# Kernel tuning notes

Measured on AMD Instinct MI355X. Metric: run time of the kernel, lower is better.

The kernel has to match this reference:

```python
import jax, jax.numpy as jnp
import numpy as np

N = 100000   # nodes
E = 3200000  # edges
F = 128      # input features
H1 = 128     # first_gcn_dimensions
H2 = 64      # second_gcn_dimensions
D1 = 64      # first_dense_neurons
D2 = 8       # second_dense_neurons
L = 10       # number_of_labels


def setup_inputs() -> dict:
    key = jax.random.key(0)
    ks = jax.random.split(key, 8)
    edges = jax.random.randint(ks[0], (2, E), 0, N)
    features = jax.random.normal(ks[1], (N, F), dtype=jnp.float32)
    s = lambda k, shape: jax.random.normal(k, shape, dtype=jnp.float32) * 0.05
    return dict(
        edges=edges, features=features,
        W1=s(ks[2], (F, H1)), b1=jnp.zeros((H1,), jnp.float32),
        W2=s(ks[3], (H1, H2)), b2=jnp.zeros((H2,), jnp.float32),
        Wf1=s(ks[4], (H2, D1)), bf1=jnp.zeros((D1,), jnp.float32),
        Wf2=s(ks[5], (D1, D2)), bf2=jnp.zeros((D2,), jnp.float32),
        Wl=s(ks[6], (H2 * D2, L)), bl=jnp.zeros((L,), jnp.float32),
    )


def gcn_conv(x, W, b, src, dst, n):
    # PyG GCNConv: x' = D^{-1/2} (A + I) D^{-1/2} (x W) + b  (self-loops already in src/dst)
    h = x @ W                                            # [N, out]
    deg = jax.ops.segment_sum(jnp.ones(dst.shape[0], x.dtype), dst, num_segments=n)
    dinv = jnp.where(deg > 0, jax.lax.rsqrt(deg), 0.0)   # deg^{-1/2}, 0 for isolated
    norm = dinv[src] * dinv[dst]                         # [E+N]
    agg = jax.ops.segment_sum(h[src] * norm[:, None], dst, num_segments=n)
    return agg + b


def reference(edges, features, W1, b1, W2, b2, Wf1, bf1, Wf2, bf2, Wl, bl):
    n = features.shape[0]
    loop = jnp.arange(n)
    src = jnp.concatenate([edges[0], loop])
    dst = jnp.concatenate([edges[1], loop])

    h1 = jax.nn.relu(gcn_conv(features, W1, b1, src, dst, n))  # [N, H1]
    h2 = gcn_conv(h1, W2, b2, src, dst, n)                     # [N, H2]

    a1 = jnp.tanh(h2 @ Wf1 + bf1)                              # [N, D1]
    att = jax.nn.softmax(a1 @ Wf2 + bf2, axis=0)               # softmax over nodes, [N, D2]

    graph_embedding = (att.T @ h2).reshape(1, -1)              # [1, D2*H2]
    P = att.T @ att - jnp.eye(att.shape[1], dtype=att.dtype)   # [D2, D2]
    penalty = jnp.sum(jnp.sqrt(jnp.sum(P * P, axis=1)))

    predictions = jax.nn.log_softmax(graph_embedding @ Wl + bl, axis=1)  # [1, L]
    return graph_embedding, penalty, predictions
```

## Files before the change

kernel.cpp:

```cpp
#include <hip/hip_runtime.h>
#include <hip/hip_bf16.h>
#include <math.h>

#define NNODES 100000
#define NEDGES 3200000
#define NBUK ((NNODES + 127) >> 7)
#define NCHUNK 256
#define EPC (NEDGES / NCHUNK)

typedef float floatx2 __attribute__((ext_vector_type(2)));
typedef float f32x4 __attribute__((ext_vector_type(4)));
typedef short bf16x8 __attribute__((ext_vector_type(8)));

__device__ __forceinline__ unsigned short f2bf(float x) {
    unsigned u = __float_as_uint(x);
    unsigned r = u + 0x7FFFu + ((u >> 16) & 1u);
    return (unsigned short)(r >> 16);
}

__device__ __forceinline__ void acc8_fp8(uint2 v, floatx2* a) {
    a[0] += __builtin_amdgcn_cvt_pk_f32_fp8(v.x, false);
    a[1] += __builtin_amdgcn_cvt_pk_f32_fp8(v.x, true);
    a[2] += __builtin_amdgcn_cvt_pk_f32_fp8(v.y, false);
    a[3] += __builtin_amdgcn_cvt_pk_f32_fp8(v.y, true);
}

__global__ void prep_w_kernel(const float* __restrict__ W1, const float* __restrict__ W2,
                              unsigned short* __restrict__ Wt1, unsigned short* __restrict__ Wt2) {
    int i = blockIdx.x * 256 + threadIdx.x;
    if (i < 128 * 128) {
        int k = i >> 7, n = i & 127;
        Wt1[n * 128 + k] = f2bf(W1[i]);
    } else if (i < 128 * 128 + 128 * 64) {
        int j = i - 128 * 128;
        int k = j >> 6, n = j & 63;
        Wt2[n * 128 + k] = f2bf(W2[j]);
    }
}

__global__ __launch_bounds__(1024) void chunk_hist_kernel(const int* __restrict__ dst,
                                                          int* __restrict__ hist) {
    __shared__ int h[NBUK];
    int c = blockIdx.x, t = threadIdx.x;
    for (int i = t; i < NBUK; i += 1024) h[i] = 0;
    __syncthreads();
    const int4* d4 = (const int4*)(dst + c * EPC);
    for (int i = t; i < EPC / 4; i += 1024) {
        int4 d = d4[i];
        atomicAdd(&h[d.x >> 7], 1);
        atomicAdd(&h[d.y >> 7], 1);
        atomicAdd(&h[d.z >> 7], 1);
        atomicAdd(&h[d.w >> 7], 1);
    }
    __syncthreads();
    for (int i = t; i < NBUK; i += 1024)
        hist[c * NBUK + i] = h[i];
}

__global__ __launch_bounds__(256) void col_scan_kernel(int* __restrict__ hist,
                                                       int* __restrict__ btot) {
    __shared__ int sdat[NCHUNK];
    int b = blockIdx.x;
    int t = threadIdx.x;
    int v = hist[t * NBUK + b];
    sdat[t] = v;
    __syncthreads();
#pragma unroll
    for (int off = 1; off < NCHUNK; off <<= 1) {
        int x = (t >= off) ? sdat[t - off] : 0;
        __syncthreads();
        sdat[t] += x;
        __syncthreads();
    }
    hist[t * NBUK + b] = sdat[t] - v;
    if (t == NCHUNK - 1) btot[b] = sdat[t];
}

__global__ void bucket_scan_kernel(const int* __restrict__ btot, int* __restrict__ bstart,
                                   int* __restrict__ row_start, float* __restrict__ smalls) {
    __shared__ int s[1024];
    int t = threadIdx.x;
    if (t < 592) smalls[t] = 0.0f;
    int v = (t < NBUK) ? btot[t] : 0;
    s[t] = v;
    __syncthreads();
    for (int off = 1; off < 1024; off <<= 1) {
        int x = (t >= off) ? s[t - off] : 0;
        __syncthreads();
        s[t] += x;
        __syncthreads();
    }
    if (t < NBUK) bstart[t] = s[t] - v;
    if (t == 0) {
        bstart[NBUK] = NEDGES;
        row_start[NNODES] = NEDGES;
    }
}

__global__ __launch_bounds__(1024) void chunk_scatter_kernel(const int* __restrict__ src,
                                                             const int* __restrict__ dst,
                                                             const int* __restrict__ hist,
                                                             const int* __restrict__ bstart,
                                                             int* __restrict__ ebuk) {
    __shared__ int cur[NBUK];
    int c = blockIdx.x, t = threadIdx.x;
    for (int i = t; i < NBUK; i += 1024)
        cur[i] = bstart[i] + hist[c * NBUK + i];
    __syncthreads();
    const int4* s4 = (const int4*)(src + c * EPC);
    const int4* d4 = (const int4*)(dst + c * EPC);
    for (int i = t; i < EPC / 4; i += 1024) {
        int4 s = s4[i];
        int4 d = d4[i];
        int p0 = atomicAdd(&cur[d.x >> 7], 1);
        ebuk[p0] = s.x | ((d.x & 127) << 20);
        int p1 = atomicAdd(&cur[d.y >> 7], 1);
        ebuk[p1] = s.y | ((d.y & 127) << 20);
        int p2 = atomicAdd(&cur[d.z >> 7], 1);
        ebuk[p2] = s.z | ((d.z & 127) << 20);
        int p3 = atomicAdd(&cur[d.w >> 7], 1);
        ebuk[p3] = s.w | ((d.w & 127) << 20);
    }
}

__global__ __launch_bounds__(256) void build_kernel(const int* __restrict__ ebuk,
                                                    const int* __restrict__ bstart,
                                                    int* __restrict__ row_start,
                                                    float* __restrict__ dinv,
                                                    int* __restrict__ csr) {
    __shared__ int cnt[128];
    __shared__ int scn[128];
    __shared__ int cur[128];
    int b = blockIdx.x;
    int t = threadIdx.x;
    int s0 = bstart[b], s1 = bstart[b + 1];
    if (t < 128) cnt[t] = 0;
    __syncthreads();
    for (int i = s0 + t; i < s1; i += 256)
        atomicAdd(&cnt[(ebuk[i] >> 20) & 127], 1);
    __syncthreads();
    if (t < 128) scn[t] = cnt[t];
    __syncthreads();
#pragma unroll
    for (int off = 1; off < 128; off <<= 1) {
        int x = (t < 128 && t >= off) ? scn[t - off] : 0;
        __syncthreads();
        if (t < 128) scn[t] += x;
        __syncthreads();
    }
    int node = b * 128 + t;
    if (t < 128) {
        int rs = s0 + scn[t] - cnt[t];
        cur[t] = rs;
        if (node < NNODES) {
            row_start[node] = rs;
            dinv[node] = rsqrtf((float)cnt[t] + 1.0f);
        }
    }
    __syncthreads();
    for (int i = s0 + t; i < s1; i += 256) {
        int v = ebuk[i];
        int pos = atomicAdd(&cur[(v >> 20) & 127], 1);
        csr[pos] = v & 0xFFFFF;
    }
}

template <int KIN, int KOUT, bool ABF16>
__global__ __launch_bounds__(256) void gemm_mfma_kernel(const void* __restrict__ Av,
                                                        const unsigned short* __restrict__ Wt,
                                                        const float* __restrict__ rowscale,
                                                        unsigned char* __restrict__ stage) {
    constexpr int LDK = KIN + 8;
    constexpr int LDC = KOUT + 4;
    constexpr int SH_AB = (64 + KOUT) * LDK * 2;
    constexpr int SH_C  = 64 * LDC * 4;
    constexpr int SH = SH_AB > SH_C ? SH_AB : SH_C;
    __shared__ char shbuf[SH];
    unsigned short* As = (unsigned short*)shbuf;
    unsigned short* Ws = As + 64 * LDK;
    float* Cs = (float*)shbuf;
    int t = threadIdx.x;
    int block_row = blockIdx.x * 64;

    for (int idx = t; idx < KOUT * (KIN / 8); idx += 256) {
        int n = idx / (KIN / 8), c = idx % (KIN / 8);
        *(uint4*)(Ws + n * LDK + c * 8) = *(const uint4*)(Wt + n * KIN + c * 8);
    }
    if (ABF16) {
        const unsigned short* A = (const unsigned short*)Av;
        for (int idx = t; idx < 64 * (KIN / 8); idx += 256) {
            int r = idx / (KIN / 8), c = idx % (KIN / 8);
            uint4 v = make_uint4(0, 0, 0, 0);
            if (block_row + r < NNODES)
                v = *(const uint4*)(A + (size_t)(block_row + r) * KIN + c * 8);
            *(uint4*)(As + r * LDK + c * 8) = v;
        }
    } else {
        const float* A = (const float*)Av;
        for (int idx = t; idx < 64 * (KIN / 4); idx += 256) {
            int r = idx / (KIN / 4), c = idx % (KIN / 4);
            float4 v = make_float4(0.f, 0.f, 0.f, 0.f);
            if (block_row + r < NNODES)
                v = *(const float4*)(A + (size_t)(block_row + r) * KIN + c * 4);
            unsigned p0 = (unsigned)f2bf(v.x) | ((unsigned)f2bf(v.y) << 16);
            unsigned p1 = (unsigned)f2bf(v.z) | ((unsigned)f2bf(v.w) << 16);
            *(uint2*)(As + r * LDK + c * 4) = make_uint2(p0, p1);
        }
    }
    __syncthreads();

    int wv = t >> 6, lane = t & 63;
    int r0 = wv * 16;
    int m = lane & 15, q = lane >> 4;
    constexpr int NT = KOUT / 16;
    constexpr int KS = KIN / 32;
    f32x4 acc[NT];
#pragma unroll
    for (int nt = 0; nt < NT; nt++) acc[nt] = (f32x4)(0.f);
    bf16x8 afr[KS];
#pragma unroll
    for (int ks = 0; ks < KS; ks++)
        afr[ks] = *(bf16x8*)(As + (r0 + m) * LDK + ks * 32 + q * 8);
#pragma unroll
    for (int nt = 0; nt < NT; nt++) {
#pragma unroll
        for (int ks = 0; ks < KS; ks++) {
            bf16x8 b = *(bf16x8*)(Ws + (nt * 16 + m) * LDK + ks * 32 + q * 8);
            acc[nt] = __builtin_amdgcn_mfma_f32_16x16x32_bf16(afr[ks], b, acc[nt], 0, 0, 0);
        }
    }
    __syncthreads();
#pragma unroll
    for (int nt = 0; nt < NT; nt++)
#pragma unroll
        for (int j = 0; j < 4; j++)
            Cs[(r0 + q * 4 + j) * LDC + nt * 16 + m] = acc[nt][j];
    __syncthreads();
    for (int idx = t; idx < 64 * (KOUT / 4); idx += 256) {
        int r = idx / (KOUT / 4), c4 = idx % (KOUT / 4);
        int row = block_row + r;
        if (row < NNODES) {
            float4 v = *(float4*)(Cs + r * LDC + c4 * 4);
            float d = rowscale[row];
            int pk = __builtin_amdgcn_cvt_pk_fp8_f32(v.x * d, v.y * d, 0, false);
            pk = __builtin_amdgcn_cvt_pk_fp8_f32(v.z * d, v.w * d, pk, true);
            *(unsigned*)(stage + (size_t)row * KOUT + c4 * 4) = (unsigned)pk;
        }
    }
}

__global__ __launch_bounds__(256) void gather128_kernel(
    const unsigned char* __restrict__ hs, const int* __restrict__ row_start,
    const int* __restrict__ csr, const float* __restrict__ dinv,
    const float* __restrict__ bias, unsigned short* __restrict__ out) {
    int wave = threadIdx.x >> 6;
    int lane = threadIdx.x & 63;
    int n = blockIdx.x * 4 + wave;
    if (n >= NNODES) return;
    int g = lane >> 4;
    int c = lane & 15;
    unsigned boff = (unsigned)c << 3;
    int start = row_start[n], end = row_start[n + 1];
    floatx2 acc[4];
#pragma unroll
    for (int i = 0; i < 4; i++) acc[i] = (floatx2)(0.f);
    int w = (start + 3) & ~3;
    if (w > end) w = end;
    {
        int e2 = start + g;
        if (e2 < w) {
            unsigned o = ((unsigned)csr[e2] << 7) + boff;
            acc8_fp8(*(const uint2*)(hs + o), acc);
        }
    }
    for (; w + 64 <= end; w += 64) {
        const int* cp = csr + w + 16 * g;
        int4 ca = *(const int4*)(cp);
        int4 cb = *(const int4*)(cp + 4);
        int4 cc = *(const int4*)(cp + 8);
        int4 cd = *(const int4*)(cp + 12);
        uint2 v0  = *(const uint2*)(hs + (((unsigned)ca.x << 7) + boff));
        uint2 v1  = *(const uint2*)(hs + (((unsigned)ca.y << 7) + boff));
        uint2 v2  = *(const uint2*)(hs + (((unsigned)ca.z << 7) + boff));
        uint2 v3  = *(const uint2*)(hs + (((unsigned)ca.w << 7) + boff));
        uint2 v4  = *(const uint2*)(hs + (((unsigned)cb.x << 7) + boff));
        uint2 v5  = *(const uint2*)(hs + (((unsigned)cb.y << 7) + boff));
        uint2 v6  = *(const uint2*)(hs + (((unsigned)cb.z << 7) + boff));
        uint2 v7  = *(const uint2*)(hs + (((unsigned)cb.w << 7) + boff));
        uint2 v8  = *(const uint2*)(hs + (((unsigned)cc.x << 7) + boff));
        uint2 v9  = *(const uint2*)(hs + (((unsigned)cc.y << 7) + boff));
        uint2 v10 = *(const uint2*)(hs + (((unsigned)cc.z << 7) + boff));
        uint2 v11 = *(const uint2*)(hs + (((unsigned)cc.w << 7) + boff));
        uint2 v12 = *(const uint2*)(hs + (((unsigned)cd.x << 7) + boff));
        uint2 v13 = *(const uint2*)(hs + (((unsigned)cd.y << 7) + boff));
        uint2 v14 = *(const uint2*)(hs + (((unsigned)cd.z << 7) + boff));
        uint2 v15 = *(const uint2*)(hs + (((unsigned)cd.w << 7) + boff));
        acc8_fp8(v0, acc);  acc8_fp8(v1, acc);  acc8_fp8(v2, acc);  acc8_fp8(v3, acc);
        acc8_fp8(v4, acc);  acc8_fp8(v5, acc);  acc8_fp8(v6, acc);  acc8_fp8(v7, acc);
        acc8_fp8(v8, acc);  acc8_fp8(v9, acc);  acc8_fp8(v10, acc); acc8_fp8(v11, acc);
        acc8_fp8(v12, acc); acc8_fp8(v13, acc); acc8_fp8(v14, acc); acc8_fp8(v15, acc);
    }
    for (; w + 16 <= end; w += 16) {
        int4 cs = *(const int4*)(csr + w + 4 * g);
        uint2 v0 = *(const uint2*)(hs + (((unsigned)cs.x << 7) + boff));
        uint2 v1 = *(const uint2*)(hs + (((unsigned)cs.y << 7) + boff));
        uint2 v2 = *(const uint2*)(hs + (((unsigned)cs.z << 7) + boff));
        uint2 v3 = *(const uint2*)(hs + (((unsigned)cs.w << 7) + boff));
        acc8_fp8(v0, acc); acc8_fp8(v1, acc); acc8_fp8(v2, acc); acc8_fp8(v3, acc);
    }
    for (int e2 = w + g; e2 < end; e2 += 4) {
        unsigned o = ((unsigned)csr[e2] << 7) + boff;
        acc8_fp8(*(const uint2*)(hs + o), acc);
    }
#pragma unroll
    for (int off = 16; off <= 32; off <<= 1)
#pragma unroll
        for (int i = 0; i < 4; i++) {
            acc[i].x += __shfl_xor(acc[i].x, off);
            acc[i].y += __shfl_xor(acc[i].y, off);
        }
    if (g == 0) {
        floatx2 s[4];
#pragma unroll
        for (int i = 0; i < 4; i++) s[i] = (floatx2)(0.f);
        acc8_fp8(*(const uint2*)(hs + (((unsigned)n << 7) + boff)), s);
        float d = dinv[n];
        int j = c * 8;
        float4 b0 = *(const float4*)(bias + j);
        float4 b1 = *(const float4*)(bias + j + 4);
        float r0 = fmaxf((acc[0].x + s[0].x) * d + b0.x, 0.f);
        float r1 = fmaxf((acc[0].y + s[0].y) * d + b0.y, 0.f);
        float r2 = fmaxf((acc[1].x + s[1].x) * d + b0.z, 0.f);
        float r3 = fmaxf((acc[1].y + s[1].y) * d + b0.w, 0.f);
        float r4 = fmaxf((acc[2].x + s[2].x) * d + b1.x, 0.f);
        float r5 = fmaxf((acc[2].y + s[2].y) * d + b1.y, 0.f);
        float r6 = fmaxf((acc[3].x + s[3].x) * d + b1.z, 0.f);
        float r7 = fmaxf((acc[3].y + s[3].y) * d + b1.w, 0.f);
        uint4 p;
        p.x = (unsigned)f2bf(r0) | ((unsigned)f2bf(r1) << 16);
        p.y = (unsigned)f2bf(r2) | ((unsigned)f2bf(r3) << 16);
        p.z = (unsigned)f2bf(r4) | ((unsigned)f2bf(r5) << 16);
        p.w = (unsigned)f2bf(r6) | ((unsigned)f2bf(r7) << 16);
        *(uint4*)(out + (((size_t)n << 7) + j)) = p;
    }
}

__global__ __launch_bounds__(256) void gather64_kernel(
    const unsigned char* __restrict__ hs, const int* __restrict__ row_start,
    const int* __restrict__ csr, const float* __restrict__ dinv,
    const float* __restrict__ bias, float* __restrict__ out) {
    int wave = threadIdx.x >> 6;
    int lane = threadIdx.x & 63;
    int n = blockIdx.x * 4 + wave;
    if (n >= NNODES) return;
    int g = lane >> 3;
    int c = lane & 7;
    unsigned boff = (unsigned)c << 3;
    int start = row_start[n], end = row_start[n + 1];
    floatx2 acc[4];
#pragma unroll
    for (int i = 0; i < 4; i++) acc[i] = (floatx2)(0.f);
    int w = (start + 3) & ~3;
    if (w > end) w = end;
    {
        int e2 = start + g;
        if (e2 < w) {
            unsigned o = ((unsigned)csr[e2] << 6) + boff;
            acc8_fp8(*(const uint2*)(hs + o), acc);
        }
    }
    for (; w + 64 <= end; w += 64) {
        const int* cp = csr + w + 8 * g;
        int4 ca = *(const int4*)(cp);
        int4 cb = *(const int4*)(cp + 4);
        uint2 v0 = *(const uint2*)(hs + (((unsigned)ca.x << 6) + boff));
        uint2 v1 = *(const uint2*)(hs + (((unsigned)ca.y << 6) + boff));
        uint2 v2 = *(const uint2*)(hs + (((unsigned)ca.z << 6) + boff));
        uint2 v3 = *(const uint2*)(hs + (((unsigned)ca.w << 6) + boff));
        uint2 v4 = *(const uint2*)(hs + (((unsigned)cb.x << 6) + boff));
        uint2 v5 = *(const uint2*)(hs + (((unsigned)cb.y << 6) + boff));
        uint2 v6 = *(const uint2*)(hs + (((unsigned)cb.z << 6) + boff));
        uint2 v7 = *(const uint2*)(hs + (((unsigned)cb.w << 6) + boff));
        acc8_fp8(v0, acc); acc8_fp8(v1, acc); acc8_fp8(v2, acc); acc8_fp8(v3, acc);
        acc8_fp8(v4, acc); acc8_fp8(v5, acc); acc8_fp8(v6, acc); acc8_fp8(v7, acc);
    }
    for (; w + 16 <= end; w += 16) {
        int2 cs = *(const int2*)(csr + w + 2 * g);
        uint2 v0 = *(const uint2*)(hs + (((unsigned)cs.x << 6) + boff));
        uint2 v1 = *(const uint2*)(hs + (((unsigned)cs.y << 6) + boff));
        acc8_fp8(v0, acc); acc8_fp8(v1, acc);
    }
    for (int e2 = w + g; e2 < end; e2 += 8) {
        unsigned o = ((unsigned)csr[e2] << 6) + boff;
        acc8_fp8(*(const uint2*)(hs + o), acc);
    }
#pragma unroll
    for (int off = 8; off <= 32; off <<= 1)
#pragma unroll
        for (int i = 0; i < 4; i++) {
            acc[i].x += __shfl_xor(acc[i].x, off);
            acc[i].y += __shfl_xor(acc[i].y, off);
        }
    if (g == 0) {
        floatx2 s[4];
#pragma unroll
        for (int i = 0; i < 4; i++) s[i] = (floatx2)(0.f);
        acc8_fp8(*(const uint2*)(hs + (((unsigned)n << 6) + boff)), s);
        float d = dinv[n];
        int j = c * 8;
        float4 b0 = *(const float4*)(bias + j);
        float4 b1 = *(const float4*)(bias + j + 4);
        float4 o0, o1;
        o0.x = (acc[0].x + s[0].x) * d + b0.x;
        o0.y = (acc[0].y + s[0].y) * d + b0.y;
        o0.z = (acc[1].x + s[1].x) * d + b0.z;
        o0.w = (acc[1].y + s[1].y) * d + b0.w;
        o1.x = (acc[2].x + s[2].x) * d + b1.x;
        o1.y = (acc[2].y + s[2].y) * d + b1.y;
        o1.z = (acc[3].x + s[3].x) * d + b1.z;
        o1.w = (acc[3].y + s[3].y) * d + b1.w;
        float* op = out + (((size_t)n << 6) + j);
        *(float4*)op = o0;
        *(float4*)(op + 4) = o1;
    }
}

__global__ __launch_bounds__(256) void attnpool_kernel(const float* __restrict__ h2,
                                                       const float* __restrict__ Wf1,
                                                       const float* __restrict__ bf1,
                                                       const float* __restrict__ Wf2,
                                                       const float* __restrict__ bf2,
                                                       float* __restrict__ ge,
                                                       float* __restrict__ ata,
                                                       float* __restrict__ colsum) {
    __shared__ float h2S[64][68];
    __shared__ float a1S[64][68];
    __shared__ float attS[64][8];
    __shared__ float colS[8][64];
    int t = threadIdx.x;
    int d0 = t >> 6;
    int j  = t & 63;
    int de = t >> 3, ee = t & 7;
    float accge0 = 0.f, accge1 = 0.f, accata = 0.f, acccol = 0.f;
    int ntiles = (NNODES + 63) / 64;
    for (int tile = blockIdx.x; tile < ntiles; tile += gridDim.x) {
        int base = tile * 64;
#pragma unroll
        for (int q = 0; q < 4; q++) {
            int idx = t + q * 256;
            int r = idx >> 4, cc = (idx & 15) * 4;
            int row = base + r;
            float4 v = (row < NNODES) ? *(const float4*)(h2 + (size_t)row * 64 + cc)
                                      : make_float4(0.f, 0.f, 0.f, 0.f);
            *(float4*)(&h2S[r][cc]) = v;
        }
        __syncthreads();
        {
            int cg = t & 15, rg = t >> 4;
            int jj = cg * 4, r0 = rg * 4;
            float4 b4 = *(const float4*)(bf1 + jj);
            float4 acc[4];
#pragma unroll
            for (int r = 0; r < 4; r++) acc[r] = b4;
#pragma unroll 4
            for (int k = 0; k < 64; k++) {
                float4 wv = *(const float4*)(Wf1 + (size_t)k * 64 + jj);
#pragma unroll
                for (int r = 0; r < 4; r++) {
                    float a = h2S[r0 + r][k];
                    acc[r].x += a * wv.x; acc[r].y += a * wv.y;
                    acc[r].z += a * wv.z; acc[r].w += a * wv.w;
                }
            }
#pragma unroll
            for (int r = 0; r < 4; r++) {
                a1S[r0 + r][jj]     = tanhf(acc[r].x);
                a1S[r0 + r][jj + 1] = tanhf(acc[r].y);
                a1S[r0 + r][jj + 2] = tanhf(acc[r].z);
                a1S[r0 + r][jj + 3] = tanhf(acc[r].w);
            }
        }
        __syncthreads();
        {
            int cc = t & 7, r = t >> 3;
#pragma unroll
            for (int h = 0; h < 2; h++) {
                int rr = r + h * 32;
                float acc = bf2[cc];
                for (int k = 0; k < 64; k++)
                    acc += a1S[rr][k] * Wf2[(size_t)k * 8 + cc];
                float ev = (base + rr < NNODES) ? __expf(acc) : 0.f;
                attS[rr][cc] = ev;
                colS[cc][rr] = ev;
            }
        }
        __syncthreads();
#pragma unroll 8
        for (int i = 0; i < 64; i++) {
            float hv = h2S[i][j];
            accge0 += attS[i][d0] * hv;
            accge1 += attS[i][d0 + 4] * hv;
        }
        if (t < 64) {
#pragma unroll 8
            for (int i = 0; i < 64; i++) accata += attS[i][de] * attS[i][ee];
        }
        if (t < 8) {
            float s = 0.f;
#pragma unroll
            for (int r = 0; r < 64; r++) s += colS[t][r];
            acccol += s;
        }
        __syncthreads();
    }
    atomicAdd(ge + d0 * 64 + j, accge0);
    atomicAdd(ge + (d0 + 4) * 64 + j, accge1);
    if (t < 64) atomicAdd(ata + de * 8 + ee, accata);
    if (t < 8) atomicAdd(colsum + t, acccol);
}

__global__ void final_kernel(const float* __restrict__ geacc, const float* __restrict__ ata,
                             const float* __restrict__ colsum, const float* __restrict__ Wl,
                             const float* __restrict__ bl, float* __restrict__ out) {
    __shared__ float geF[512];
    __shared__ float inv[8];
    __shared__ float logits[10];
    int t = threadIdx.x;
    if (t < 8) inv[t] = 1.0f / colsum[t];
    __syncthreads();
    for (int idx = t; idx < 512; idx += 64) {
        int d = idx >> 6;
        float v = geacc[idx] * inv[d];
        geF[idx] = v;
        out[idx] = v;
    }
    __syncthreads();
    if (t == 0) {
        float pen = 0.f;
        for (int d = 0; d < 8; d++) {
            float s = 0.f;
            for (int e = 0; e < 8; e++) {
                float p = ata[d * 8 + e] * inv[d] * inv[e] - (d == e ? 1.0f : 0.0f);
                s += p * p;
            }
            pen += sqrtf(s);
        }
        out[512] = pen;
    }
    if (t < 10) {
        float acc = bl[t];
        for (int k = 0; k < 512; k++) acc += geF[k] * Wl[(size_t)k * 10 + t];
        logits[t] = acc;
    }
    __syncthreads();
    if (t == 0) {
        float m = -INFINITY;
        for (int l = 0; l < 10; l++) m = fmaxf(m, logits[l]);
        float s = 0.f;
        for (int l = 0; l < 10; l++) s += expf(logits[l] - m);
        float ls = logf(s);
        for (int l = 0; l < 10; l++) out[513 + l] = logits[l] - m - ls;
    }
}

extern "C" void kernel_launch(void* const* d_in, const int* in_sizes, int n_in,
                              void* d_out, int out_size, void* d_ws, size_t ws_size,
                              hipStream_t stream) {
    const int* esrc = (const int*)d_in[0];
    const int* edst = esrc + NEDGES;
    const float* X   = (const float*)d_in[1];
    const float* W1  = (const float*)d_in[2];
    const float* b1  = (const float*)d_in[3];
    const float* W2  = (const float*)d_in[4];
    const float* b2  = (const float*)d_in[5];
    const float* Wf1 = (const float*)d_in[6];
    const float* bf1 = (const float*)d_in[7];
    const float* Wf2 = (const float*)d_in[8];
    const float* bf2 = (const float*)d_in[9];
    const float* Wl  = (const float*)d_in[10];
    const float* bl  = (const float*)d_in[11];
    float* out = (float*)d_out;

    float* ws     = (float*)d_ws;
    float* dinv   = ws;
    float* smalls = ws + 100352;
    float* colsum = smalls + 8;
    float* ata    = smalls + 16;
    float* geacc  = smalls + 80;
    float* A = ws + 101376;
    float* B = A + (size_t)NNODES * 128;
    int* row_start = (int*)(B + (size_t)NNODES * 128);
    int* btot      = row_start + 100352;
    int* bstart    = btot + 1024;
    int* csr       = bstart + 1024;
    unsigned short* Wt1 = (unsigned short*)(csr + NEDGES);
    unsigned short* Wt2 = Wt1 + 128 * 128;
    int* ebuk      = (int*)A;
    int* hist      = (int*)B;
    unsigned char* stage = (unsigned char*)A;
    unsigned short* h1 = (unsigned short*)B;
    float* h2  = B;

    prep_w_kernel<<<96, 256, 0, stream>>>(W1, W2, Wt1, Wt2);

    chunk_hist_kernel<<<NCHUNK, 1024, 0, stream>>>(edst, hist);
    col_scan_kernel<<<NBUK, 256, 0, stream>>>(hist, btot);
    bucket_scan_kernel<<<1, 1024, 0, stream>>>(btot, bstart, row_start, smalls);
    chunk_scatter_kernel<<<NCHUNK, 1024, 0, stream>>>(esrc, edst, hist, bstart, ebuk);
    build_kernel<<<NBUK, 256, 0, stream>>>(ebuk, bstart, row_start, dinv, csr);

    gemm_mfma_kernel<128, 128, false><<<(NNODES + 63) / 64, 256, 0, stream>>>(X, Wt1, dinv, stage);
    gather128_kernel<<<(NNODES + 3) / 4, 256, 0, stream>>>(stage, row_start, csr, dinv, b1, h1);

    gemm_mfma_kernel<128, 64, true><<<(NNODES + 63) / 64, 256, 0, stream>>>(h1, Wt2, dinv, stage);
    gather64_kernel<<<(NNODES + 3) / 4, 256, 0, stream>>>(stage, row_start, csr, dinv, b2, h2);

    attnpool_kernel<<<512, 256, 0, stream>>>(h2, Wf1, bf1, Wf2, bf2, geacc, ata, colsum);
    final_kernel<<<1, 64, 0, stream>>>(geacc, ata, colsum, Wl, bl, out);
}
```

Baseline: 421.4 us.

## Split first-layer fp8 staging into two 64-column slices and gather per slice

The first GEMM now writes its fp8 output as two column slices of 64 bytes per row instead of one 128-byte row. The first-layer gather launches twice as many blocks, each handling one slice, with 8 edge groups of 8 lanes instead of 4 groups of 16. The aim is to shrink the random-access working set per pass so each slice fits better in cache, and to raise memory-level parallelism per wave. In exchange, the CSR indices and row offsets are read twice, and the per-row gathers become 64-byte accesses.

```diff
diff --git a/kernel.cpp b/kernel.cpp
--- a/kernel.cpp
+++ b/kernel.cpp
@@ -7,6 +7,8 @@
 #define NBUK ((NNODES + 127) >> 7)
 #define NCHUNK 256
 #define EPC (NEDGES / NCHUNK)
+#define NPAD 100352
+#define SLICE1B ((size_t)NPAD * 64)
 
 typedef float floatx2 __attribute__((ext_vector_type(2)));
 typedef float f32x4 __attribute__((ext_vector_type(4)));
@@ -244,21 +246,28 @@
             float d = rowscale[row];
             int pk = __builtin_amdgcn_cvt_pk_fp8_f32(v.x * d, v.y * d, 0, false);
             pk = __builtin_amdgcn_cvt_pk_fp8_f32(v.z * d, v.w * d, pk, true);
-            *(unsigned*)(stage + (size_t)row * KOUT + c4 * 4) = (unsigned)pk;
-        }
-    }
-}
-
-__global__ __launch_bounds__(256) void gather128_kernel(
+            if constexpr (KOUT == 128) {
+                *(unsigned*)(stage + (size_t)(c4 >> 4) * SLICE1B
+                                   + ((size_t)row << 6) + ((c4 & 15) << 2)) = (unsigned)pk;
+            } else {
+                *(unsigned*)(stage + (size_t)row * KOUT + c4 * 4) = (unsigned)pk;
+            }
+        }
+    }
+}
+
+__global__ __launch_bounds__(256) void gather128s_kernel(
     const unsigned char* __restrict__ hs, const int* __restrict__ row_start,
     const int* __restrict__ csr, const float* __restrict__ dinv,
     const float* __restrict__ bias, unsigned short* __restrict__ out) {
     int wave = threadIdx.x >> 6;
     int lane = threadIdx.x & 63;
-    int n = blockIdx.x * 4 + wave;
+    int s = (int)(blockIdx.x & 1);
+    int n = (int)(blockIdx.x >> 1) * 4 + wave;
     if (n >= NNODES) return;
-    int g = lane >> 4;
-    int c = lane & 15;
+    int g = lane >> 3;
+    int c = lane & 7;
+    const unsigned char* hss = hs + (size_t)s * SLICE1B;
     unsigned boff = (unsigned)c << 3;
     int start = row_start[n], end = row_start[n + 1];
     floatx2 acc[4];
@@ -269,73 +278,59 @@
     {
         int e2 = start + g;
         if (e2 < w) {
-            unsigned o = ((unsigned)csr[e2] << 7) + boff;
-            acc8_fp8(*(const uint2*)(hs + o), acc);
+            unsigned o = ((unsigned)csr[e2] << 6) + boff;
+            acc8_fp8(*(const uint2*)(hss + o), acc);
         }
     }
     for (; w + 64 <= end; w += 64) {
-        const int* cp = csr + w + 16 * g;
+        const int* cp = csr + w + 8 * g;
         int4 ca = *(const int4*)(cp);
         int4 cb = *(const int4*)(cp + 4);
-        int4 cc = *(const int4*)(cp + 8);
-        int4 cd = *(const int4*)(cp + 12);
-        uint2 v0  = *(const uint2*)(hs + (((unsigned)ca.x << 7) + boff));
-        uint2 v1  = *(const uint2*)(hs + (((unsigned)ca.y << 7) + boff));
-        uint2 v2  = *(const uint2*)(hs + (((unsigned)ca.z << 7) + boff));
-        uint2 v3  = *(const uint2*)(hs + (((unsigned)ca.w << 7) + boff));
-        uint2 v4  = *(const uint2*)(hs + (((unsigned)cb.x << 7) + boff));
-        uint2 v5  = *(const uint2*)(hs + (((unsigned)cb.y << 7) + boff));
-        uint2 v6  = *(const uint2*)(hs + (((unsigned)cb.z << 7) + boff));
-        uint2 v7  = *(const uint2*)(hs + (((unsigned)cb.w << 7) + boff));
-        uint2 v8  = *(const uint2*)(hs + (((unsigned)cc.x << 7) + boff));
-        uint2 v9  = *(const uint2*)(hs + (((unsigned)cc.y << 7) + boff));
-        uint2 v10 = *(const uint2*)(hs + (((unsigned)cc.z << 7) + boff));
-        uint2 v11 = *(const uint2*)(hs + (((unsigned)cc.w << 7) + boff));
-        uint2 v12 = *(const uint2*)(hs + (((unsigned)cd.x << 7) + boff));
-        uint2 v13 = *(const uint2*)(hs + (((unsigned)cd.y << 7) + boff));
-        uint2 v14 = *(const uint2*)(hs + (((unsigned)cd.z << 7) + boff));
-        uint2 v15 = *(const uint2*)(hs + (((unsigned)cd.w << 7) + boff));
-        acc8_fp8(v0, acc);  acc8_fp8(v1, acc);  acc8_fp8(v2, acc);  acc8_fp8(v3, acc);
-        acc8_fp8(v4, acc);  acc8_fp8(v5, acc);  acc8_fp8(v6, acc);  acc8_fp8(v7, acc);
-        acc8_fp8(v8, acc);  acc8_fp8(v9, acc);  acc8_fp8(v10, acc); acc8_fp8(v11, acc);
-        acc8_fp8(v12, acc); acc8_fp8(v13, acc); acc8_fp8(v14, acc); acc8_fp8(v15, acc);
+        uint2 v0 = *(const uint2*)(hss + (((unsigned)ca.x << 6) + boff));
+        uint2 v1 = *(const uint2*)(hss + (((unsigned)ca.y << 6) + boff));
+        uint2 v2 = *(const uint2*)(hss + (((unsigned)ca.z << 6) + boff));
+        uint2 v3 = *(const uint2*)(hss + (((unsigned)ca.w << 6) + boff));
+        uint2 v4 = *(const uint2*)(hss + (((unsigned)cb.x << 6) + boff));
+        uint2 v5 = *(const uint2*)(hss + (((unsigned)cb.y << 6) + boff));
+        uint2 v6 = *(const uint2*)(hss + (((unsigned)cb.z << 6) + boff));
+        uint2 v7 = *(const uint2*)(hss + (((unsigned)cb.w << 6) + boff));
+        acc8_fp8(v0, acc); acc8_fp8(v1, acc); acc8_fp8(v2, acc); acc8_fp8(v3, acc);
+        acc8_fp8(v4, acc); acc8_fp8(v5, acc); acc8_fp8(v6, acc); acc8_fp8(v7, acc);
     }
     for (; w + 16 <= end; w += 16) {
-        int4 cs = *(const int4*)(csr + w + 4 * g);
-        uint2 v0 = *(const uint2*)(hs + (((unsigned)cs.x << 7) + boff));
-        uint2 v1 = *(const uint2*)(hs + (((unsigned)cs.y << 7) + boff));
-        uint2 v2 = *(const uint2*)(hs + (((unsigned)cs.z << 7) + boff));
-        uint2 v3 = *(const uint2*)(hs + (((unsigned)cs.w << 7) + boff));
-        acc8_fp8(v0, acc); acc8_fp8(v1, acc); acc8_fp8(v2, acc); acc8_fp8(v3, acc);
-    }
-    for (int e2 = w + g; e2 < end; e2 += 4) {
-        unsigned o = ((unsigned)csr[e2] << 7) + boff;
-        acc8_fp8(*(const uint2*)(hs + o), acc);
-    }
-#pragma unroll
-    for (int off = 16; off <= 32; off <<= 1)
+        int2 cs = *(const int2*)(csr + w + 2 * g);
+        uint2 v0 = *(const uint2*)(hss + (((unsigned)cs.x << 6) + boff));
+        uint2 v1 = *(const uint2*)(hss + (((unsigned)cs.y << 6) + boff));
+        acc8_fp8(v0, acc); acc8_fp8(v1, acc);
+    }
+    for (int e2 = w + g; e2 < end; e2 += 8) {
+        unsigned o = ((unsigned)csr[e2] << 6) + boff;
+        acc8_fp8(*(const uint2*)(hss + o), acc);
+    }
+#pragma unroll
+    for (int off = 8; off <= 32; off <<= 1)
 #pragma unroll
         for (int i = 0; i < 4; i++) {
             acc[i].x += __shfl_xor(acc[i].x, off);
             acc[i].y += __shfl_xor(acc[i].y, off);
         }
     if (g == 0) {
-        floatx2 s[4];
-#pragma unroll
-        for (int i = 0; i < 4; i++) s[i] = (floatx2)(0.f);
-        acc8_fp8(*(const uint2*)(hs + (((unsigned)n << 7) + boff)), s);
+        floatx2 sf[4];
+#pragma unroll
+        for (int i = 0; i < 4; i++) sf[i] = (floatx2)(0.f);
+        acc8_fp8(*(const uint2*)(hss + (((unsigned)n << 6) + boff)), sf);
         float d = dinv[n];
-        int j = c * 8;
+        int j = s * 64 + c * 8;
         float4 b0 = *(const float4*)(bias + j);
         float4 b1 = *(const float4*)(bias + j + 4);
-        float r0 = fmaxf((acc[0].x + s[0].x) * d + b0.x, 0.f);
-        float r1 = fmaxf((acc[0].y + s[0].y) * d + b0.y, 0.f);
-        float r2 = fmaxf((acc[1].x + s[1].x) * d + b0.z, 0.f);
-        float r3 = fmaxf((acc[1].y + s[1].y) * d + b0.w, 0.f);
-        float r4 = fmaxf((acc[2].x + s[2].x) * d + b1.x, 0.f);
-        float r5 = fmaxf((acc[2].y + s[2].y) * d + b1.y, 0.f);
-        float r6 = fmaxf((acc[3].x + s[3].x) * d + b1.z, 0.f);
-        float r7 = fmaxf((acc[3].y + s[3].y) * d + b1.w, 0.f);
+        float r0 = fmaxf((acc[0].x + sf[0].x) * d + b0.x, 0.f);
+        float r1 = fmaxf((acc[0].y + sf[0].y) * d + b0.y, 0.f);
+        float r2 = fmaxf((acc[1].x + sf[1].x) * d + b0.z, 0.f);
+        float r3 = fmaxf((acc[1].y + sf[1].y) * d + b0.w, 0.f);
+        float r4 = fmaxf((acc[2].x + sf[2].x) * d + b1.x, 0.f);
+        float r5 = fmaxf((acc[2].y + sf[2].y) * d + b1.y, 0.f);
+        float r6 = fmaxf((acc[3].x + sf[3].x) * d + b1.z, 0.f);
+        float r7 = fmaxf((acc[3].y + sf[3].y) * d + b1.w, 0.f);
         uint4 p;
         p.x = (unsigned)f2bf(r0) | ((unsigned)f2bf(r1) << 16);
         p.y = (unsigned)f2bf(r2) | ((unsigned)f2bf(r3) << 16);
@@ -610,7 +605,7 @@
     build_kernel<<<NBUK, 256, 0, stream>>>(ebuk, bstart, row_start, dinv, csr);
 
     gemm_mfma_kernel<128, 128, false><<<(NNODES + 63) / 64, 256, 0, stream>>>(X, Wt1, dinv, stage);
-    gather128_kernel<<<(NNODES + 3) / 4, 256, 0, stream>>>(stage, row_start, csr, dinv, b1, h1);
+    gather128s_kernel<<<((NNODES + 3) / 4) * 2, 256, 0, stream>>>(stage, row_start, csr, dinv, b1, h1);
 
     gemm_mfma_kernel<128, 64, true><<<(NNODES + 63) / 64, 256, 0, stream>>>(h1, Wt2, dinv, stage);
     gather64_kernel<<<(NNODES + 3) / 4, 256, 0, stream>>>(stage, row_start, csr, dinv, b2, h2);
```

Result: slower. 459.8 us (+9.1%).
